# Kernel optimization log

Hardware: AMD Instinct MI355X
Metric: run time of the kernel (lower is better)

The kernel has to match this reference:

```python
import jax, jax.numpy as jnp
import numpy as np

N, E, H, NIN, DD = 10000, 160000, 128, 128, 256
SCALE = 30.0
EPS = 1e-5

def _ln(x, g, b):
    mu = jnp.mean(x, axis=-1, keepdims=True)
    var = jnp.mean((x - mu) ** 2, axis=-1, keepdims=True)
    return (x - mu) * jax.lax.rsqrt(var + EPS) * g + b

def _gelu(x):
    return jax.nn.gelu(x, approximate=False)  # torch nn.GELU default (erf)

def setup_inputs() -> dict:
    key = jax.random.key(0)
    ks = jax.random.split(key, 16)
    def w(k, i, o):
        return jax.random.normal(k, (i, o), jnp.float32) * (1.0 / np.sqrt(i))
    return {
        "h_V": jax.random.normal(ks[0], (N, H), jnp.float32),
        "h_E": jax.random.normal(ks[1], (E, H + NIN), jnp.float32),
        "edge_idx": jax.random.randint(ks[2], (2, E), 0, N, jnp.int32),
        # message MLP: (H+NIN)->H, H->H
        "m_w0": w(ks[3], H + NIN, H), "m_b0": jnp.zeros((H,), jnp.float32),
        "m_w1": w(ks[4], H, H),       "m_b1": jnp.zeros((H,), jnp.float32),
        # dense MLP: H->DD, DD->DD, final DD->H
        "d_w0": w(ks[5], H, DD),  "d_b0": jnp.zeros((DD,), jnp.float32),
        "d_w1": w(ks[6], DD, DD), "d_b1": jnp.zeros((DD,), jnp.float32),
        "d_w2": w(ks[7], DD, H),  "d_b2": jnp.zeros((H,), jnp.float32),
        # LayerNorm params
        "g1": jnp.ones((H,), jnp.float32), "be1": jnp.zeros((H,), jnp.float32),
        "g2": jnp.ones((H,), jnp.float32), "be2": jnp.zeros((H,), jnp.float32),
    }

def reference(h_V, h_E, edge_idx, m_w0, m_b0, m_w1, m_b1,
              d_w0, d_b0, d_w1, d_b1, d_w2, d_b2, g1, be1, g2, be2):
    src_idx = edge_idx[0]
    # message MLP over edges (dropout = identity at inference)
    h = _gelu(h_E @ m_w0 + m_b0)
    h_message = _gelu(h @ m_w1 + m_b1)          # [E, H]
    # scatter-sum aggregate edges -> nodes
    dh = jax.ops.segment_sum(h_message, src_idx, num_segments=N) / SCALE
    h_V = _ln(h_V + dh, g1, be1)
    # dense MLP over nodes
    d = _gelu(h_V @ d_w0 + d_b0)
    d = _gelu(d @ d_w1 + d_b1)
    dh = d @ d_w2 + d_b2
    return _ln(h_V + dh, g2, be2)
```

## Files before the change

### kernel.cpp

```cpp
#include <hip/hip_runtime.h>
#include <hip/hip_bf16.h>


typedef __attribute__((ext_vector_type(8))) short bf16x8;
typedef __attribute__((ext_vector_type(4))) float f32x4;

__device__ __forceinline__ unsigned short f2bf(float f) {
  union { float f; unsigned u; } v; v.f = f;
  return (unsigned short)((v.u + 0x7fffu + ((v.u >> 16) & 1u)) >> 16);
}
__device__ __forceinline__ unsigned pk2bf(float a, float b) {
  __hip_bfloat162 h = __float22bfloat162_rn(make_float2(a, b));
  union { __hip_bfloat162 h; unsigned u; } v; v.h = h;
  return v.u;
}
__device__ __forceinline__ unsigned short bf1(float x) {
  return (unsigned short)pk2bf(x, x);
}
__device__ __forceinline__ float bf2f(unsigned s) {
  union { unsigned u; float f; } v; v.u = s << 16;
  return v.f;
}
__device__ __forceinline__ float gelu_f(float x) {
  float x2 = x * x;
  float u2 = x * fmaf(0.0713548162f, x2, 1.5957691216f);
  float e = __expf(u2);
  float r = __builtin_amdgcn_rcpf(e + 1.0f);
  float th = fmaf(-2.0f, r, 1.0f);
  float hx = 0.5f * x;
  return fmaf(hx, th, hx);
}

__global__ void k_pack(const float* __restrict__ mw0, const float* __restrict__ mw1,
                       const float* __restrict__ dw0, const float* __restrict__ dw1,
                       const float* __restrict__ dw2,
                       unsigned short* __restrict__ pw0, unsigned short* __restrict__ pw1,
                       unsigned short* __restrict__ pd0, unsigned short* __restrict__ pd1,
                       unsigned short* __restrict__ pd2,
                       int* __restrict__ counts, int Nn) {
  int g = blockIdx.x, lane = threadIdx.x;
  int z = g * 64 + lane;
  if (z < Nn) counts[z] = 0;
  const float* src; unsigned short* dst; int K, N, WC, base;
  if (g < 64)       { src = mw0; dst = pw0; K = 256; N = 128; WC = 128; base = 0; }
  else if (g < 96)  { src = mw1; dst = pw1; K = 128; N = 128; WC = 128; base = 64; }
  else if (g < 160) { src = dw0; dst = pd0; K = 128; N = 256; WC = 64; base = 96; }
  else if (g < 288) { src = dw1; dst = pd1; K = 256; N = 256; WC = 64; base = 160; }
  else              { src = dw2; dst = pd2; K = 256; N = 128; WC = 32; base = 288; }
  int lg = g - base;
  int KS = K >> 5, CTKS = (WC >> 4) * KS;
  int w = lg / CTKS, rem = lg % CTKS, ct = rem / KS, ks = rem % KS;
  int col = w * WC + ct * 16 + (lane & 15);
  int k0 = ks * 32 + (lane >> 4) * 8;
  unsigned short o[8];
#pragma unroll
  for (int j = 0; j < 8; ++j) o[j] = f2bf(src[(size_t)(k0 + j) * N + col]);
  uint4 u;
  u.x = (unsigned)o[0] | ((unsigned)o[1] << 16);
  u.y = (unsigned)o[2] | ((unsigned)o[3] << 16);
  u.z = (unsigned)o[4] | ((unsigned)o[5] << 16);
  u.w = (unsigned)o[6] | ((unsigned)o[7] << 16);
  *(uint4*)(dst + (size_t)(lg * 64 + lane) * 8) = u;
}

__global__ void k_hist(const int* __restrict__ eidx, int* __restrict__ counts, int E) {
  int e = blockIdx.x * 256 + threadIdx.x;
  if (e < E) atomicAdd(&counts[eidx[e]], 1);
}

__global__ __launch_bounds__(1024) void k_scan(const int* __restrict__ counts,
                                               int* __restrict__ row_start,
                                               int* __restrict__ cursor, int Nn) {
  __shared__ int sm[1024];
  int t = threadIdx.x;
  int chunk = (Nn + 1023) / 1024;
  int lo = t * chunk, hi = lo + chunk;
  if (hi > Nn) hi = Nn;
  int s = 0;
  for (int i = lo; i < hi; ++i) s += counts[i];
  sm[t] = s;
  __syncthreads();
  for (int o = 1; o < 1024; o <<= 1) {
    int u = (t >= o) ? sm[t - o] : 0;
    __syncthreads();
    sm[t] += u;
    __syncthreads();
  }
  int run = sm[t] - s;
  for (int i = lo; i < hi; ++i) {
    row_start[i] = run; cursor[i] = run; run += counts[i];
  }
  if (t == 1023) row_start[Nn] = sm[1023];
}

__global__ void k_scatter(const int* __restrict__ eidx, int* __restrict__ cursor,
                          int* __restrict__ eorder, int E) {
  int e = blockIdx.x * 256 + threadIdx.x;
  if (e < E) {
    int pos = atomicAdd(&cursor[eidx[e]], 1);
    eorder[pos] = e;
  }
}

__global__ __launch_bounds__(512, 2) void k_edge(
    const float* __restrict__ hE, const unsigned short* __restrict__ pw0,
    const unsigned short* __restrict__ pw1, const float* __restrict__ b0,
    const float* __restrict__ b1, unsigned short* __restrict__ hmsg, int E) {
  __shared__ __align__(16) char lds[131072];
  const int tid = threadIdx.x;
  const int wid = tid >> 6, lane = tid & 63;
  const int l15 = lane & 15, lhi = lane >> 4;
  char* Hw = lds + 98304 + wid * 4096;

  {
    const uint4* s0 = (const uint4*)pw0;
    const uint4* s1 = (const uint4*)pw1;
    uint4* d = (uint4*)lds;
#pragma unroll
    for (int i = 0; i < 12; ++i) {
      int idx = i * 512 + tid;
      d[idx] = (idx < 4096) ? s0[idx] : s1[idx - 4096];
    }
  }
  float bb0[8], bb1[8];
#pragma unroll
  for (int ct = 0; ct < 8; ++ct) {
    bb0[ct] = b0[ct * 16 + l15];
    bb1[ct] = b1[ct * 16 + l15];
  }
  __syncthreads();

  const int TILES = (E + 15) >> 4;
  const int WSLOTS = gridDim.x * 8;
  int t = blockIdx.x * 8 + wid;
  if (t >= TILES) return;

  f32x4 av[16];
  {
    int rowA = t * 16 + l15; rowA = rowA < E ? rowA : E - 1;
    const float* ap = hE + (size_t)rowA * 256 + lhi * 8;
#pragma unroll
    for (int ks = 0; ks < 8; ++ks) {
      av[2 * ks]     = *(const f32x4*)(ap + ks * 32);
      av[2 * ks + 1] = *(const f32x4*)(ap + ks * 32 + 4);
    }
  }

  for (; t < TILES; t += WSLOTS) {
    const int tn = t + WSLOTS;
    bf16x8 af[8];
#pragma unroll
    for (int ks = 0; ks < 8; ++ks) {
      union { unsigned u[4]; bf16x8 v; } pk;
      pk.u[0] = pk2bf(av[2 * ks][0], av[2 * ks][1]);
      pk.u[1] = pk2bf(av[2 * ks][2], av[2 * ks][3]);
      pk.u[2] = pk2bf(av[2 * ks + 1][0], av[2 * ks + 1][1]);
      pk.u[3] = pk2bf(av[2 * ks + 1][2], av[2 * ks + 1][3]);
      af[ks] = pk.v;
    }
    if (tn < TILES) {
      int rowA = tn * 16 + l15; rowA = rowA < E ? rowA : E - 1;
      const float* ap = hE + (size_t)rowA * 256 + lhi * 8;
#pragma unroll
      for (int ks = 0; ks < 8; ++ks) {
        av[2 * ks]     = *(const f32x4*)(ap + ks * 32);
        av[2 * ks + 1] = *(const f32x4*)(ap + ks * 32 + 4);
      }
    }

    f32x4 acc[8];
#pragma unroll
    for (int ct = 0; ct < 8; ++ct) {
      float b = bb0[ct];
      acc[ct][0] = b; acc[ct][1] = b; acc[ct][2] = b; acc[ct][3] = b;
    }
#pragma unroll
    for (int ks = 0; ks < 8; ++ks) {
#pragma unroll
      for (int g = 0; g < 2; ++g) {
        bf16x8 bfr[4];
#pragma unroll
        for (int q = 0; q < 4; ++q)
          bfr[q] = *(bf16x8*)(lds + ((g * 4 + q) * 8 + ks) * 1024 + lane * 16);
        __builtin_amdgcn_s_setprio(1);
#pragma unroll
        for (int q = 0; q < 4; ++q)
          acc[g * 4 + q] =
              __builtin_amdgcn_mfma_f32_16x16x32_bf16(af[ks], bfr[q], acc[g * 4 + q], 0, 0, 0);
        __builtin_amdgcn_s_setprio(0);
      }
    }
#pragma unroll
    for (int ct = 0; ct < 8; ++ct)
#pragma unroll
      for (int j = 0; j < 4; ++j) {
        int r = lhi * 4 + j, col = ct * 16 + l15;
        *(unsigned short*)(Hw + r * 256 + ((col * 2) ^ ((r & 7) << 4))) =
            bf1(gelu_f(acc[ct][j]));
      }

    f32x4 acc2[8];
#pragma unroll
    for (int ct = 0; ct < 8; ++ct) {
      float b = bb1[ct];
      acc2[ct][0] = b; acc2[ct][1] = b; acc2[ct][2] = b; acc2[ct][3] = b;
    }
#pragma unroll
    for (int ks = 0; ks < 4; ++ks) {
      bf16x8 a = *(bf16x8*)(Hw + l15 * 256 + ((ks * 64 + lhi * 16) ^ ((l15 & 7) << 4)));
#pragma unroll
      for (int g = 0; g < 2; ++g) {
        bf16x8 bfr[4];
#pragma unroll
        for (int q = 0; q < 4; ++q)
          bfr[q] = *(bf16x8*)(lds + 65536 + ((g * 4 + q) * 4 + ks) * 1024 + lane * 16);
        __builtin_amdgcn_s_setprio(1);
#pragma unroll
        for (int q = 0; q < 4; ++q)
          acc2[g * 4 + q] =
              __builtin_amdgcn_mfma_f32_16x16x32_bf16(a, bfr[q], acc2[g * 4 + q], 0, 0, 0);
        __builtin_amdgcn_s_setprio(0);
      }
    }
    const int row0 = t * 16;
#pragma unroll
    for (int ct = 0; ct < 8; ++ct)
#pragma unroll
      for (int j = 0; j < 4; ++j) {
        int r = row0 + lhi * 4 + j;
        if (r < E) {
          int col = ct * 16 + l15;
          hmsg[(size_t)r * 128 + col] = bf1(gelu_f(acc2[ct][j]));
        }
      }
  }
}

__global__ __launch_bounds__(256) void k_aggln(
    const unsigned* __restrict__ hmsg, const float2* __restrict__ hV,
    const int* __restrict__ row_start, const int* __restrict__ eorder,
    const float* __restrict__ g1, const float* __restrict__ be1,
    float2* __restrict__ hv1f, unsigned* __restrict__ hv1b, int Nn) {
  int wid = threadIdx.x >> 6, lane = threadIdx.x & 63;
  int node = blockIdx.x * 4 + wid;
  if (node >= Nn) return;
  int s = row_start[node], e = row_start[node + 1];
  float s0 = 0.f, s1 = 0.f;
  int i = s;
  for (; i + 3 < e; i += 4) {
    int e0 = eorder[i], e1 = eorder[i + 1], e2 = eorder[i + 2], e3 = eorder[i + 3];
    unsigned v0 = hmsg[(size_t)e0 * 64 + lane];
    unsigned v1 = hmsg[(size_t)e1 * 64 + lane];
    unsigned v2 = hmsg[(size_t)e2 * 64 + lane];
    unsigned v3 = hmsg[(size_t)e3 * 64 + lane];
    s0 += bf2f(v0 & 0xffffu) + bf2f(v1 & 0xffffu) + bf2f(v2 & 0xffffu) + bf2f(v3 & 0xffffu);
    s1 += bf2f(v0 >> 16) + bf2f(v1 >> 16) + bf2f(v2 >> 16) + bf2f(v3 >> 16);
  }
  for (; i < e; ++i) {
    unsigned v = hmsg[(size_t)eorder[i] * 64 + lane];
    s0 += bf2f(v & 0xffffu);
    s1 += bf2f(v >> 16);
  }
  float2 hv = hV[(size_t)node * 64 + lane];
  float x0 = hv.x + s0 * (1.f / 30.f);
  float x1 = hv.y + s1 * (1.f / 30.f);
  float sum = x0 + x1, sq = x0 * x0 + x1 * x1;
#pragma unroll
  for (int off = 32; off > 0; off >>= 1) {
    sum += __shfl_xor(sum, off);
    sq += __shfl_xor(sq, off);
  }
  float mu = sum * (1.f / 128.f);
  float var = sq * (1.f / 128.f) - mu * mu;
  float rs = rsqrtf(var + 1e-5f);
  int c = lane * 2;
  float y0 = (x0 - mu) * rs * g1[c] + be1[c];
  float y1 = (x1 - mu) * rs * g1[c + 1] + be1[c + 1];
  hv1f[(size_t)node * 64 + lane] = make_float2(y0, y1);
  hv1b[(size_t)node * 64 + lane] = (unsigned)pk2bf(y0, y1);
}

__global__ __launch_bounds__(256, 4) void k_node(
    const unsigned short* __restrict__ xb, const unsigned short* __restrict__ pd0,
    const unsigned short* __restrict__ pd1, const unsigned short* __restrict__ pd2,
    const float* __restrict__ db0, const float* __restrict__ db1,
    const float* __restrict__ db2, const float* __restrict__ hv1f,
    const float* __restrict__ g2, const float* __restrict__ be2,
    float* __restrict__ out, int Nn) {
  __shared__ __align__(16) char lds[8192 + 16384 + 16384];
  char* A0 = lds;
  char* D0 = lds + 8192;
  char* D1 = lds + 8192 + 16384;
  float* Y = (float*)D0;
  const int tid = threadIdx.x, wid = tid >> 6, lane = tid & 63;
  const int l15 = lane & 15, lhi = lane >> 4;
  const int row0 = blockIdx.x * 32;

  {
    int idx = tid;
    int r = idx >> 3, c = idx & 7;
    uint4 v = make_uint4(0u, 0u, 0u, 0u);
    if (row0 + r < Nn) v = ((const uint4*)xb)[(size_t)(row0 + r) * 16 + c * 2];
    *(uint4*)(A0 + r * 256 + ((c * 32) ^ ((r & 7) << 4))) = v;
    uint4 v2 = make_uint4(0u, 0u, 0u, 0u);
    if (row0 + r < Nn) v2 = ((const uint4*)xb)[(size_t)(row0 + r) * 16 + c * 2 + 1];
    *(uint4*)(A0 + r * 256 + (((c * 32) + 16) ^ ((r & 7) << 4))) = v2;
  }
  __syncthreads();

  {
    f32x4 acc[2][4];
#pragma unroll
    for (int ct = 0; ct < 4; ++ct) {
      float b = db0[wid * 64 + ct * 16 + l15];
#pragma unroll
      for (int mt = 0; mt < 2; ++mt) {
        acc[mt][ct][0] = b; acc[mt][ct][1] = b; acc[mt][ct][2] = b; acc[mt][ct][3] = b;
      }
    }
#pragma unroll
    for (int ks = 0; ks < 4; ++ks) {
      bf16x8 a[2];
#pragma unroll
      for (int mt = 0; mt < 2; ++mt) {
        int row = mt * 16 + l15;
        a[mt] = *(bf16x8*)(A0 + row * 256 + ((ks * 64 + lhi * 16) ^ ((row & 7) << 4)));
      }
#pragma unroll
      for (int ct = 0; ct < 4; ++ct) {
        uint4 bv = ((const uint4*)pd0)[(size_t)(wid * 16 + ct * 4 + ks) * 64 + lane];
        bf16x8 b = *(bf16x8*)&bv;
#pragma unroll
        for (int mt = 0; mt < 2; ++mt)
          acc[mt][ct] = __builtin_amdgcn_mfma_f32_16x16x32_bf16(a[mt], b, acc[mt][ct], 0, 0, 0);
      }
    }
#pragma unroll
    for (int ct = 0; ct < 4; ++ct) {
      int col = wid * 64 + ct * 16 + l15;
#pragma unroll
      for (int mt = 0; mt < 2; ++mt)
#pragma unroll
        for (int j = 0; j < 4; ++j) {
          int r = mt * 16 + lhi * 4 + j;
          *(unsigned short*)(D0 + r * 512 + ((col * 2) ^ ((r & 7) << 4))) =
              bf1(gelu_f(acc[mt][ct][j]));
        }
    }
  }
  __syncthreads();

  {
    f32x4 acc[2][4];
#pragma unroll
    for (int ct = 0; ct < 4; ++ct) {
      float b = db1[wid * 64 + ct * 16 + l15];
#pragma unroll
      for (int mt = 0; mt < 2; ++mt) {
        acc[mt][ct][0] = b; acc[mt][ct][1] = b; acc[mt][ct][2] = b; acc[mt][ct][3] = b;
      }
    }
#pragma unroll
    for (int ks = 0; ks < 8; ++ks) {
      bf16x8 a[2];
#pragma unroll
      for (int mt = 0; mt < 2; ++mt) {
        int row = mt * 16 + l15;
        a[mt] = *(bf16x8*)(D0 + row * 512 + ((ks * 64 + lhi * 16) ^ ((row & 7) << 4)));
      }
#pragma unroll
      for (int ct = 0; ct < 4; ++ct) {
        uint4 bv = ((const uint4*)pd1)[(size_t)(wid * 32 + ct * 8 + ks) * 64 + lane];
        bf16x8 b = *(bf16x8*)&bv;
#pragma unroll
        for (int mt = 0; mt < 2; ++mt)
          acc[mt][ct] = __builtin_amdgcn_mfma_f32_16x16x32_bf16(a[mt], b, acc[mt][ct], 0, 0, 0);
      }
    }
#pragma unroll
    for (int ct = 0; ct < 4; ++ct) {
      int col = wid * 64 + ct * 16 + l15;
#pragma unroll
      for (int mt = 0; mt < 2; ++mt)
#pragma unroll
        for (int j = 0; j < 4; ++j) {
          int r = mt * 16 + lhi * 4 + j;
          *(unsigned short*)(D1 + r * 512 + ((col * 2) ^ ((r & 7) << 4))) =
              bf1(gelu_f(acc[mt][ct][j]));
        }
    }
  }
  __syncthreads();

  {
    f32x4 acc[2][2];
#pragma unroll
    for (int ct = 0; ct < 2; ++ct) {
      float b = db2[wid * 32 + ct * 16 + l15];
#pragma unroll
      for (int mt = 0; mt < 2; ++mt) {
        acc[mt][ct][0] = b; acc[mt][ct][1] = b; acc[mt][ct][2] = b; acc[mt][ct][3] = b;
      }
    }
#pragma unroll
    for (int ks = 0; ks < 8; ++ks) {
      bf16x8 a[2];
#pragma unroll
      for (int mt = 0; mt < 2; ++mt) {
        int row = mt * 16 + l15;
        a[mt] = *(bf16x8*)(D1 + row * 512 + ((ks * 64 + lhi * 16) ^ ((row & 7) << 4)));
      }
#pragma unroll
      for (int ct = 0; ct < 2; ++ct) {
        uint4 bv = ((const uint4*)pd2)[(size_t)(wid * 16 + ct * 8 + ks) * 64 + lane];
        bf16x8 b = *(bf16x8*)&bv;
#pragma unroll
        for (int mt = 0; mt < 2; ++mt)
          acc[mt][ct] = __builtin_amdgcn_mfma_f32_16x16x32_bf16(a[mt], b, acc[mt][ct], 0, 0, 0);
      }
    }
    __syncthreads();
#pragma unroll
    for (int ct = 0; ct < 2; ++ct) {
      int col = wid * 32 + ct * 16 + l15;
#pragma unroll
      for (int mt = 0; mt < 2; ++mt)
#pragma unroll
        for (int j = 0; j < 4; ++j) {
          int r = mt * 16 + lhi * 4 + j;
          int grow = row0 + r;
          float res = (grow < Nn) ? hv1f[(size_t)grow * 128 + col] : 0.f;
          Y[r * 128 + col] = acc[mt][ct][j] + res;
        }
    }
  }
  __syncthreads();

  float g2a = g2[lane * 2], g2b = g2[lane * 2 + 1];
  float ba = be2[lane * 2], bbx = be2[lane * 2 + 1];
  for (int ii = 0; ii < 8; ++ii) {
    int r = wid * 8 + ii;
    int grow = row0 + r;
    if (grow >= Nn) continue;
    float2 xy = *(float2*)&Y[r * 128 + lane * 2];
    float sum = xy.x + xy.y, sq = xy.x * xy.x + xy.y * xy.y;
#pragma unroll
    for (int off = 32; off > 0; off >>= 1) {
      sum += __shfl_xor(sum, off);
      sq += __shfl_xor(sq, off);
    }
    float mu = sum * (1.f / 128.f);
    float var = sq * (1.f / 128.f) - mu * mu;
    float rs = rsqrtf(var + 1e-5f);
    float y0 = (xy.x - mu) * rs * g2a + ba;
    float y1 = (xy.y - mu) * rs * g2b + bbx;
    *(float2*)&out[(size_t)grow * 128 + lane * 2] = make_float2(y0, y1);
  }
}

extern "C" void kernel_launch(void* const* d_in, const int* in_sizes, int n_in,
                              void* d_out, int out_size, void* d_ws, size_t ws_size,
                              hipStream_t stream) {
  const float* hV  = (const float*)d_in[0];
  const float* hE  = (const float*)d_in[1];
  const int* eidx  = (const int*)d_in[2];
  const float* mw0 = (const float*)d_in[3];
  const float* mb0 = (const float*)d_in[4];
  const float* mw1 = (const float*)d_in[5];
  const float* mb1 = (const float*)d_in[6];
  const float* dw0 = (const float*)d_in[7];
  const float* db0 = (const float*)d_in[8];
  const float* dw1 = (const float*)d_in[9];
  const float* db1 = (const float*)d_in[10];
  const float* dw2 = (const float*)d_in[11];
  const float* db2 = (const float*)d_in[12];
  const float* g1  = (const float*)d_in[13];
  const float* be1 = (const float*)d_in[14];
  const float* g2  = (const float*)d_in[15];
  const float* be2 = (const float*)d_in[16];
  const int Nn = in_sizes[0] / 128;
  const int E  = in_sizes[1] / 256;

  char* ws = (char*)d_ws;
  size_t off = 0;
  auto alloc = [&](size_t bytes) -> char* {
    off = (off + 255) & ~(size_t)255;
    char* p = ws + off;
    off += bytes;
    return p;
  };
  unsigned short* hmsg = (unsigned short*)alloc((size_t)E * 128 * 2);
  float* hv1f          = (float*)alloc((size_t)Nn * 128 * 4);
  unsigned short* hv1b = (unsigned short*)alloc((size_t)Nn * 128 * 2);
  unsigned short* pw0  = (unsigned short*)alloc(32768 * 2);
  unsigned short* pw1  = (unsigned short*)alloc(16384 * 2);
  unsigned short* pd0  = (unsigned short*)alloc(32768 * 2);
  unsigned short* pd1  = (unsigned short*)alloc(65536 * 2);
  unsigned short* pd2  = (unsigned short*)alloc(32768 * 2);
  int* counts    = (int*)alloc((size_t)Nn * 4);
  int* row_start = (int*)alloc((size_t)(Nn + 1) * 4);
  int* cursor    = (int*)alloc((size_t)Nn * 4);
  int* eorder    = (int*)alloc((size_t)E * 4);

  k_pack<<<352, 64, 0, stream>>>(mw0, mw1, dw0, dw1, dw2, pw0, pw1, pd0, pd1, pd2,
                                 counts, Nn);
  k_hist<<<(E + 255) / 256, 256, 0, stream>>>(eidx, counts, E);
  k_scan<<<1, 1024, 0, stream>>>(counts, row_start, cursor, Nn);
  k_scatter<<<(E + 255) / 256, 256, 0, stream>>>(eidx, cursor, eorder, E);
  k_edge<<<256, 512, 0, stream>>>(hE, pw0, pw1, mb0, mb1, hmsg, E);
  k_aggln<<<(Nn + 3) / 4, 256, 0, stream>>>((const unsigned*)hmsg, (const float2*)hV,
                                            row_start, eorder, g1, be1,
                                            (float2*)hv1f, (unsigned*)hv1b, Nn);
  const int nt = (Nn + 31) / 32;
  k_node<<<nt, 256, 0, stream>>>(hv1b, pd0, pd1, pd2, db0, db1, db2,
                                 hv1f, g2, be2, (float*)d_out, Nn);
}
```

Before: 131.2 us.

## Split fused edge MLP into two kernels with a global intermediate buffer

The fused two-layer edge MLP kernel is split into k_edge1 (first GEMM plus GELU, written to a new global bf16 buffer) and k_edge2 (second GEMM plus GELU reading that buffer). Each kernel now needs less LDS, and k_edge1 launches twice as many blocks, so the intent is higher occupancy and more parallelism. The software prefetch of the next tile's input is also removed. The cost is an extra round trip of E x 128 bf16 through global memory (about 40 MB of traffic) plus one more kernel launch.

```diff
diff --git a/kernel.cpp b/kernel.cpp
--- a/kernel.cpp
+++ b/kernel.cpp
@@ -102,69 +102,47 @@
   }
 }
 
-__global__ __launch_bounds__(512, 2) void k_edge(
+__global__ __launch_bounds__(512, 2) void k_edge1(
     const float* __restrict__ hE, const unsigned short* __restrict__ pw0,
-    const unsigned short* __restrict__ pw1, const float* __restrict__ b0,
-    const float* __restrict__ b1, unsigned short* __restrict__ hmsg, int E) {
-  __shared__ __align__(16) char lds[131072];
+    const float* __restrict__ b0, unsigned short* __restrict__ Hg, int E) {
+  __shared__ __align__(16) char lds[65536];
   const int tid = threadIdx.x;
   const int wid = tid >> 6, lane = tid & 63;
   const int l15 = lane & 15, lhi = lane >> 4;
-  char* Hw = lds + 98304 + wid * 4096;
 
   {
     const uint4* s0 = (const uint4*)pw0;
-    const uint4* s1 = (const uint4*)pw1;
     uint4* d = (uint4*)lds;
 #pragma unroll
-    for (int i = 0; i < 12; ++i) {
-      int idx = i * 512 + tid;
-      d[idx] = (idx < 4096) ? s0[idx] : s1[idx - 4096];
-    }
-  }
-  float bb0[8], bb1[8];
-#pragma unroll
-  for (int ct = 0; ct < 8; ++ct) {
-    bb0[ct] = b0[ct * 16 + l15];
-    bb1[ct] = b1[ct * 16 + l15];
-  }
+    for (int i = 0; i < 8; ++i) d[i * 512 + tid] = s0[i * 512 + tid];
+  }
+  float bb0[8];
+#pragma unroll
+  for (int ct = 0; ct < 8; ++ct) bb0[ct] = b0[ct * 16 + l15];
   __syncthreads();
 
   const int TILES = (E + 15) >> 4;
   const int WSLOTS = gridDim.x * 8;
-  int t = blockIdx.x * 8 + wid;
-  if (t >= TILES) return;
-
-  f32x4 av[16];
-  {
+  for (int t = blockIdx.x * 8 + wid; t < TILES; t += WSLOTS) {
     int rowA = t * 16 + l15; rowA = rowA < E ? rowA : E - 1;
     const float* ap = hE + (size_t)rowA * 256 + lhi * 8;
-#pragma unroll
-    for (int ks = 0; ks < 8; ++ks) {
-      av[2 * ks]     = *(const f32x4*)(ap + ks * 32);
-      av[2 * ks + 1] = *(const f32x4*)(ap + ks * 32 + 4);
-    }
-  }
-
-  for (; t < TILES; t += WSLOTS) {
-    const int tn = t + WSLOTS;
+
     bf16x8 af[8];
-#pragma unroll
-    for (int ks = 0; ks < 8; ++ks) {
-      union { unsigned u[4]; bf16x8 v; } pk;
-      pk.u[0] = pk2bf(av[2 * ks][0], av[2 * ks][1]);
-      pk.u[1] = pk2bf(av[2 * ks][2], av[2 * ks][3]);
-      pk.u[2] = pk2bf(av[2 * ks + 1][0], av[2 * ks + 1][1]);
-      pk.u[3] = pk2bf(av[2 * ks + 1][2], av[2 * ks + 1][3]);
-      af[ks] = pk.v;
-    }
-    if (tn < TILES) {
-      int rowA = tn * 16 + l15; rowA = rowA < E ? rowA : E - 1;
-      const float* ap = hE + (size_t)rowA * 256 + lhi * 8;
+    {
+      f32x4 av[16];
 #pragma unroll
       for (int ks = 0; ks < 8; ++ks) {
         av[2 * ks]     = *(const f32x4*)(ap + ks * 32);
         av[2 * ks + 1] = *(const f32x4*)(ap + ks * 32 + 4);
+      }
+#pragma unroll
+      for (int ks = 0; ks < 8; ++ks) {
+        union { unsigned u[4]; bf16x8 v; } pk;
+        pk.u[0] = pk2bf(av[2 * ks][0], av[2 * ks][1]);
+        pk.u[1] = pk2bf(av[2 * ks][2], av[2 * ks][3]);
+        pk.u[2] = pk2bf(av[2 * ks + 1][0], av[2 * ks + 1][1]);
+        pk.u[3] = pk2bf(av[2 * ks + 1][2], av[2 * ks + 1][3]);
+        af[ks] = pk.v;
       }
     }
 
@@ -190,38 +168,6 @@
         __builtin_amdgcn_s_setprio(0);
       }
     }
-#pragma unroll
-    for (int ct = 0; ct < 8; ++ct)
-#pragma unroll
-      for (int j = 0; j < 4; ++j) {
-        int r = lhi * 4 + j, col = ct * 16 + l15;
-        *(unsigned short*)(Hw + r * 256 + ((col * 2) ^ ((r & 7) << 4))) =
-            bf1(gelu_f(acc[ct][j]));
-      }
-
-    f32x4 acc2[8];
-#pragma unroll
-    for (int ct = 0; ct < 8; ++ct) {
-      float b = bb1[ct];
-      acc2[ct][0] = b; acc2[ct][1] = b; acc2[ct][2] = b; acc2[ct][3] = b;
-    }
-#pragma unroll
-    for (int ks = 0; ks < 4; ++ks) {
-      bf16x8 a = *(bf16x8*)(Hw + l15 * 256 + ((ks * 64 + lhi * 16) ^ ((l15 & 7) << 4)));
-#pragma unroll
-      for (int g = 0; g < 2; ++g) {
-        bf16x8 bfr[4];
-#pragma unroll
-        for (int q = 0; q < 4; ++q)
-          bfr[q] = *(bf16x8*)(lds + 65536 + ((g * 4 + q) * 4 + ks) * 1024 + lane * 16);
-        __builtin_amdgcn_s_setprio(1);
-#pragma unroll
-        for (int q = 0; q < 4; ++q)
-          acc2[g * 4 + q] =
-              __builtin_amdgcn_mfma_f32_16x16x32_bf16(a, bfr[q], acc2[g * 4 + q], 0, 0, 0);
-        __builtin_amdgcn_s_setprio(0);
-      }
-    }
     const int row0 = t * 16;
 #pragma unroll
     for (int ct = 0; ct < 8; ++ct)
@@ -230,7 +176,74 @@
         int r = row0 + lhi * 4 + j;
         if (r < E) {
           int col = ct * 16 + l15;
-          hmsg[(size_t)r * 128 + col] = bf1(gelu_f(acc2[ct][j]));
+          Hg[(size_t)r * 128 + col] = bf1(gelu_f(acc[ct][j]));
+        }
+      }
+  }
+}
+
+__global__ __launch_bounds__(256, 4) void k_edge2(
+    const unsigned short* __restrict__ Hg, const unsigned short* __restrict__ pw1,
+    const float* __restrict__ b1, unsigned short* __restrict__ hmsg, int E) {
+  __shared__ __align__(16) char lds[32768];
+  const int tid = threadIdx.x;
+  const int wid = tid >> 6, lane = tid & 63;
+  const int l15 = lane & 15, lhi = lane >> 4;
+
+  {
+    const uint4* s1 = (const uint4*)pw1;
+    uint4* d = (uint4*)lds;
+#pragma unroll
+    for (int i = 0; i < 8; ++i) d[i * 256 + tid] = s1[i * 256 + tid];
+  }
+  float bb1[8];
+#pragma unroll
+  for (int ct = 0; ct < 8; ++ct) bb1[ct] = b1[ct * 16 + l15];
+  __syncthreads();
+
+  const int TILES = (E + 15) >> 4;
+  const int WSLOTS = gridDim.x * 4;
+  for (int t = blockIdx.x * 4 + wid; t < TILES; t += WSLOTS) {
+    int rowA = t * 16 + l15; rowA = rowA < E ? rowA : E - 1;
+    const unsigned short* ap = Hg + (size_t)rowA * 128 + lhi * 8;
+
+    bf16x8 af[4];
+#pragma unroll
+    for (int ks = 0; ks < 4; ++ks) {
+      uint4 v = *(const uint4*)(ap + ks * 32);
+      af[ks] = *(bf16x8*)&v;
+    }
+    f32x4 acc[8];
+#pragma unroll
+    for (int ct = 0; ct < 8; ++ct) {
+      float b = bb1[ct];
+      acc[ct][0] = b; acc[ct][1] = b; acc[ct][2] = b; acc[ct][3] = b;
+    }
+#pragma unroll
+    for (int ks = 0; ks < 4; ++ks) {
+#pragma unroll
+      for (int g = 0; g < 2; ++g) {
+        bf16x8 bfr[4];
+#pragma unroll
+        for (int q = 0; q < 4; ++q)
+          bfr[q] = *(bf16x8*)(lds + ((g * 4 + q) * 4 + ks) * 1024 + lane * 16);
+        __builtin_amdgcn_s_setprio(1);
+#pragma unroll
+        for (int q = 0; q < 4; ++q)
+          acc[g * 4 + q] =
+              __builtin_amdgcn_mfma_f32_16x16x32_bf16(af[ks], bfr[q], acc[g * 4 + q], 0, 0, 0);
+        __builtin_amdgcn_s_setprio(0);
+      }
+    }
+    const int row0 = t * 16;
+#pragma unroll
+    for (int ct = 0; ct < 8; ++ct)
+#pragma unroll
+      for (int j = 0; j < 4; ++j) {
+        int r = row0 + lhi * 4 + j;
+        if (r < E) {
+          int col = ct * 16 + l15;
+          hmsg[(size_t)r * 128 + col] = bf1(gelu_f(acc[ct][j]));
         }
       }
   }
@@ -490,6 +503,7 @@
     return p;
   };
   unsigned short* hmsg = (unsigned short*)alloc((size_t)E * 128 * 2);
+  unsigned short* Hg   = (unsigned short*)alloc((size_t)E * 128 * 2);
   float* hv1f          = (float*)alloc((size_t)Nn * 128 * 4);
   unsigned short* hv1b = (unsigned short*)alloc((size_t)Nn * 128 * 2);
   unsigned short* pw0  = (unsigned short*)alloc(32768 * 2);
@@ -507,7 +521,8 @@
   k_hist<<<(E + 255) / 256, 256, 0, stream>>>(eidx, counts, E);
   k_scan<<<1, 1024, 0, stream>>>(counts, row_start, cursor, Nn);
   k_scatter<<<(E + 255) / 256, 256, 0, stream>>>(eidx, cursor, eorder, E);
-  k_edge<<<256, 512, 0, stream>>>(hE, pw0, pw1, mb0, mb1, hmsg, E);
+  k_edge1<<<512, 512, 0, stream>>>(hE, pw0, mb0, Hg, E);
+  k_edge2<<<1024, 256, 0, stream>>>(Hg, pw1, mb1, hmsg, E);
   k_aggln<<<(Nn + 3) / 4, 256, 0, stream>>>((const unsigned*)hmsg, (const float2*)hV,
                                             row_start, eorder, g1, be1,
                                             (float2*)hv1f, (unsigned*)hv1b, Nn);
```

New measurement: 209.3 us. +59.6%, slower.

## Switch edge MLP to 32x32x16 MFMA tiles with 32-row edge tiles

Applied to the files above, without the earlier changes.

Repacks the message-MLP weights for the 32x32 MFMA fragment layout and rewrites the edge kernel to process 32 edges per wave using mfma_f32_32x32x16_bf16. This halves the number of B-fragment LDS reads per output and reduces instruction count per FLOP. It drops the cross-iteration prefetch of the next tile's h_E, loading the two K halves within the iteration instead. It also raises LDS to 160KB per block, which could limit the 2-blocks-per-CU occupancy and increases register pressure.

```diff
diff --git a/kernel.cpp b/kernel.cpp
--- a/kernel.cpp
+++ b/kernel.cpp
@@ -4,6 +4,7 @@
 
 typedef __attribute__((ext_vector_type(8))) short bf16x8;
 typedef __attribute__((ext_vector_type(4))) float f32x4;
+typedef __attribute__((ext_vector_type(16))) float f32x16;
 
 __device__ __forceinline__ unsigned short f2bf(float f) {
   union { float f; unsigned u; } v; v.f = f;
@@ -41,10 +42,26 @@
   int g = blockIdx.x, lane = threadIdx.x;
   int z = g * 64 + lane;
   if (z < Nn) counts[z] = 0;
+  unsigned short o[8];
+  if (g < 96) {
+    const float* src; unsigned short* dst; int lg;
+    int ct, kstep;
+    if (g < 64) { src = mw0; dst = pw0; lg = g; ct = lg >> 4; kstep = lg & 15; }
+    else        { src = mw1; dst = pw1; lg = g - 64; ct = lg >> 3; kstep = lg & 7; }
+    int col = ct * 32 + (lane & 31);
+    int k0 = kstep * 16 + (lane >> 5) * 8;
+#pragma unroll
+    for (int j = 0; j < 8; ++j) o[j] = f2bf(src[(size_t)(k0 + j) * 128 + col]);
+    uint4 u;
+    u.x = (unsigned)o[0] | ((unsigned)o[1] << 16);
+    u.y = (unsigned)o[2] | ((unsigned)o[3] << 16);
+    u.z = (unsigned)o[4] | ((unsigned)o[5] << 16);
+    u.w = (unsigned)o[6] | ((unsigned)o[7] << 16);
+    *(uint4*)(dst + (size_t)(lg * 64 + lane) * 8) = u;
+    return;
+  }
   const float* src; unsigned short* dst; int K, N, WC, base;
-  if (g < 64)       { src = mw0; dst = pw0; K = 256; N = 128; WC = 128; base = 0; }
-  else if (g < 96)  { src = mw1; dst = pw1; K = 128; N = 128; WC = 128; base = 64; }
-  else if (g < 160) { src = dw0; dst = pd0; K = 128; N = 256; WC = 64; base = 96; }
+  if (g < 160)      { src = dw0; dst = pd0; K = 128; N = 256; WC = 64; base = 96; }
   else if (g < 288) { src = dw1; dst = pd1; K = 256; N = 256; WC = 64; base = 160; }
   else              { src = dw2; dst = pd2; K = 256; N = 128; WC = 32; base = 288; }
   int lg = g - base;
@@ -52,7 +69,6 @@
   int w = lg / CTKS, rem = lg % CTKS, ct = rem / KS, ks = rem % KS;
   int col = w * WC + ct * 16 + (lane & 15);
   int k0 = ks * 32 + (lane >> 4) * 8;
-  unsigned short o[8];
 #pragma unroll
   for (int j = 0; j < 8; ++j) o[j] = f2bf(src[(size_t)(k0 + j) * N + col]);
   uint4 u;
@@ -106,11 +122,11 @@
     const float* __restrict__ hE, const unsigned short* __restrict__ pw0,
     const unsigned short* __restrict__ pw1, const float* __restrict__ b0,
     const float* __restrict__ b1, unsigned short* __restrict__ hmsg, int E) {
-  __shared__ __align__(16) char lds[131072];
+  __shared__ __align__(16) char lds[163840];
   const int tid = threadIdx.x;
   const int wid = tid >> 6, lane = tid & 63;
-  const int l15 = lane & 15, lhi = lane >> 4;
-  char* Hw = lds + 98304 + wid * 4096;
+  const int l31 = lane & 31, lsel = lane >> 5;
+  char* Hw = lds + 98304 + wid * 8192;
 
   {
     const uint4* s0 = (const uint4*)pw0;
@@ -122,115 +138,130 @@
       d[idx] = (idx < 4096) ? s0[idx] : s1[idx - 4096];
     }
   }
-  float bb0[8], bb1[8];
-#pragma unroll
-  for (int ct = 0; ct < 8; ++ct) {
-    bb0[ct] = b0[ct * 16 + l15];
-    bb1[ct] = b1[ct * 16 + l15];
+  float bb0[4], bb1[4];
+#pragma unroll
+  for (int ct = 0; ct < 4; ++ct) {
+    bb0[ct] = b0[ct * 32 + l31];
+    bb1[ct] = b1[ct * 32 + l31];
   }
   __syncthreads();
 
-  const int TILES = (E + 15) >> 4;
+  const int TILES = (E + 31) >> 5;
   const int WSLOTS = gridDim.x * 8;
-  int t = blockIdx.x * 8 + wid;
-  if (t >= TILES) return;
-
-  f32x4 av[16];
-  {
-    int rowA = t * 16 + l15; rowA = rowA < E ? rowA : E - 1;
-    const float* ap = hE + (size_t)rowA * 256 + lhi * 8;
-#pragma unroll
-    for (int ks = 0; ks < 8; ++ks) {
-      av[2 * ks]     = *(const f32x4*)(ap + ks * 32);
-      av[2 * ks + 1] = *(const f32x4*)(ap + ks * 32 + 4);
-    }
-  }
-
-  for (; t < TILES; t += WSLOTS) {
-    const int tn = t + WSLOTS;
+  for (int t = blockIdx.x * 8 + wid; t < TILES; t += WSLOTS) {
+    int rowA = t * 32 + l31; rowA = rowA < E ? rowA : E - 1;
+    const float* ap = hE + (size_t)rowA * 256 + lsel * 8;
+
     bf16x8 af[8];
-#pragma unroll
-    for (int ks = 0; ks < 8; ++ks) {
+    {
+      f32x4 av[16];
+#pragma unroll
+      for (int kk = 0; kk < 8; ++kk) {
+        av[2 * kk]     = *(const f32x4*)(ap + kk * 16);
+        av[2 * kk + 1] = *(const f32x4*)(ap + kk * 16 + 4);
+      }
+#pragma unroll
+      for (int kk = 0; kk < 8; ++kk) {
+        union { unsigned u[4]; bf16x8 v; } pk;
+        pk.u[0] = pk2bf(av[2 * kk][0], av[2 * kk][1]);
+        pk.u[1] = pk2bf(av[2 * kk][2], av[2 * kk][3]);
+        pk.u[2] = pk2bf(av[2 * kk + 1][0], av[2 * kk + 1][1]);
+        pk.u[3] = pk2bf(av[2 * kk + 1][2], av[2 * kk + 1][3]);
+        af[kk] = pk.v;
+      }
+    }
+    f32x4 av1[16];
+#pragma unroll
+    for (int kk = 0; kk < 8; ++kk) {
+      av1[2 * kk]     = *(const f32x4*)(ap + 128 + kk * 16);
+      av1[2 * kk + 1] = *(const f32x4*)(ap + 128 + kk * 16 + 4);
+    }
+
+    f32x16 acc[4];
+#pragma unroll
+    for (int ct = 0; ct < 4; ++ct) {
+      float b = bb0[ct];
+#pragma unroll
+      for (int q = 0; q < 16; ++q) acc[ct][q] = b;
+    }
+#pragma unroll
+    for (int kk = 0; kk < 8; ++kk) {
+      bf16x8 bfr[4];
+#pragma unroll
+      for (int ct = 0; ct < 4; ++ct)
+        bfr[ct] = *(bf16x8*)(lds + (ct * 16 + kk) * 1024 + lane * 16);
+      __builtin_amdgcn_s_setprio(1);
+#pragma unroll
+      for (int ct = 0; ct < 4; ++ct)
+        acc[ct] = __builtin_amdgcn_mfma_f32_32x32x16_bf16(af[kk], bfr[ct], acc[ct], 0, 0, 0);
+      __builtin_amdgcn_s_setprio(0);
+    }
+#pragma unroll
+    for (int kk = 0; kk < 8; ++kk) {
       union { unsigned u[4]; bf16x8 v; } pk;
-      pk.u[0] = pk2bf(av[2 * ks][0], av[2 * ks][1]);
-      pk.u[1] = pk2bf(av[2 * ks][2], av[2 * ks][3]);
-      pk.u[2] = pk2bf(av[2 * ks + 1][0], av[2 * ks + 1][1]);
-      pk.u[3] = pk2bf(av[2 * ks + 1][2], av[2 * ks + 1][3]);
-      af[ks] = pk.v;
-    }
-    if (tn < TILES) {
-      int rowA = tn * 16 + l15; rowA = rowA < E ? rowA : E - 1;
-      const float* ap = hE + (size_t)rowA * 256 + lhi * 8;
-#pragma unroll
-      for (int ks = 0; ks < 8; ++ks) {
-        av[2 * ks]     = *(const f32x4*)(ap + ks * 32);
-        av[2 * ks + 1] = *(const f32x4*)(ap + ks * 32 + 4);
-      }
-    }
-
-    f32x4 acc[8];
-#pragma unroll
-    for (int ct = 0; ct < 8; ++ct) {
-      float b = bb0[ct];
-      acc[ct][0] = b; acc[ct][1] = b; acc[ct][2] = b; acc[ct][3] = b;
-    }
-#pragma unroll
-    for (int ks = 0; ks < 8; ++ks) {
-#pragma unroll
-      for (int g = 0; g < 2; ++g) {
-        bf16x8 bfr[4];
-#pragma unroll
-        for (int q = 0; q < 4; ++q)
-          bfr[q] = *(bf16x8*)(lds + ((g * 4 + q) * 8 + ks) * 1024 + lane * 16);
-        __builtin_amdgcn_s_setprio(1);
-#pragma unroll
-        for (int q = 0; q < 4; ++q)
-          acc[g * 4 + q] =
-              __builtin_amdgcn_mfma_f32_16x16x32_bf16(af[ks], bfr[q], acc[g * 4 + q], 0, 0, 0);
-        __builtin_amdgcn_s_setprio(0);
-      }
-    }
-#pragma unroll
-    for (int ct = 0; ct < 8; ++ct)
-#pragma unroll
-      for (int j = 0; j < 4; ++j) {
-        int r = lhi * 4 + j, col = ct * 16 + l15;
-        *(unsigned short*)(Hw + r * 256 + ((col * 2) ^ ((r & 7) << 4))) =
-            bf1(gelu_f(acc[ct][j]));
-      }
-
-    f32x4 acc2[8];
-#pragma unroll
-    for (int ct = 0; ct < 8; ++ct) {
+      pk.u[0] = pk2bf(av1[2 * kk][0], av1[2 * kk][1]);
+      pk.u[1] = pk2bf(av1[2 * kk][2], av1[2 * kk][3]);
+      pk.u[2] = pk2bf(av1[2 * kk + 1][0], av1[2 * kk + 1][1]);
+      pk.u[3] = pk2bf(av1[2 * kk + 1][2], av1[2 * kk + 1][3]);
+      af[kk] = pk.v;
+    }
+#pragma unroll
+    for (int kk = 0; kk < 8; ++kk) {
+      bf16x8 bfr[4];
+#pragma unroll
+      for (int ct = 0; ct < 4; ++ct)
+        bfr[ct] = *(bf16x8*)(lds + (ct * 16 + 8 + kk) * 1024 + lane * 16);
+      __builtin_amdgcn_s_setprio(1);
+#pragma unroll
+      for (int ct = 0; ct < 4; ++ct)
+        acc[ct] = __builtin_amdgcn_mfma_f32_32x32x16_bf16(af[kk], bfr[ct], acc[ct], 0, 0, 0);
+      __builtin_amdgcn_s_setprio(0);
+    }
+
+#pragma unroll
+    for (int ct = 0; ct < 4; ++ct)
+#pragma unroll
+      for (int reg = 0; reg < 16; ++reg) {
+        int row = (reg & 3) + 8 * (reg >> 2) + 4 * lsel;
+        int col = ct * 32 + l31;
+        *(unsigned short*)(Hw + row * 256 + ((col * 2) ^ ((row & 7) << 4))) =
+            bf1(gelu_f(acc[ct][reg]));
+      }
+
+    f32x16 acc2[4];
+#pragma unroll
+    for (int ct = 0; ct < 4; ++ct) {
       float b = bb1[ct];
-      acc2[ct][0] = b; acc2[ct][1] = b; acc2[ct][2] = b; acc2[ct][3] = b;
-    }
-#pragma unroll
-    for (int ks = 0; ks < 4; ++ks) {
-      bf16x8 a = *(bf16x8*)(Hw + l15 * 256 + ((ks * 64 + lhi * 16) ^ ((l15 & 7) << 4)));
-#pragma unroll
-      for (int g = 0; g < 2; ++g) {
-        bf16x8 bfr[4];
-#pragma unroll
-        for (int q = 0; q < 4; ++q)
-          bfr[q] = *(bf16x8*)(lds + 65536 + ((g * 4 + q) * 4 + ks) * 1024 + lane * 16);
-        __builtin_amdgcn_s_setprio(1);
-#pragma unroll
-        for (int q = 0; q < 4; ++q)
-          acc2[g * 4 + q] =
-              __builtin_amdgcn_mfma_f32_16x16x32_bf16(a, bfr[q], acc2[g * 4 + q], 0, 0, 0);
-        __builtin_amdgcn_s_setprio(0);
-      }
-    }
-    const int row0 = t * 16;
-#pragma unroll
-    for (int ct = 0; ct < 8; ++ct)
-#pragma unroll
-      for (int j = 0; j < 4; ++j) {
-        int r = row0 + lhi * 4 + j;
+#pragma unroll
+      for (int q = 0; q < 16; ++q) acc2[ct][q] = b;
+    }
+    bf16x8 a2[8];
+#pragma unroll
+    for (int kk = 0; kk < 8; ++kk)
+      a2[kk] = *(bf16x8*)(Hw + l31 * 256 +
+                          ((kk * 32 + lsel * 16) ^ ((l31 & 7) << 4)));
+#pragma unroll
+    for (int kk = 0; kk < 8; ++kk) {
+      bf16x8 bfr[4];
+#pragma unroll
+      for (int ct = 0; ct < 4; ++ct)
+        bfr[ct] = *(bf16x8*)(lds + 65536 + (ct * 8 + kk) * 1024 + lane * 16);
+      __builtin_amdgcn_s_setprio(1);
+#pragma unroll
+      for (int ct = 0; ct < 4; ++ct)
+        acc2[ct] = __builtin_amdgcn_mfma_f32_32x32x16_bf16(a2[kk], bfr[ct], acc2[ct], 0, 0, 0);
+      __builtin_amdgcn_s_setprio(0);
+    }
+
+    const int row0 = t * 32;
+#pragma unroll
+    for (int ct = 0; ct < 4; ++ct)
+#pragma unroll
+      for (int reg = 0; reg < 16; ++reg) {
+        int r = row0 + (reg & 3) + 8 * (reg >> 2) + 4 * lsel;
         if (r < E) {
-          int col = ct * 16 + l15;
-          hmsg[(size_t)r * 128 + col] = bf1(gelu_f(acc2[ct][j]));
+          int col = ct * 32 + l31;
+          hmsg[(size_t)r * 128 + col] = bf1(gelu_f(acc2[ct][reg]));
         }
       }
   }
```

Result: slower. 210.3 us (+60.3%).
